# Kernel optimization log

Hardware: AMD Instinct MI355X
Metric: run time of the kernel (lower is better)

The kernel has to match this reference:

```python
import jax, jax.numpy as jnp
import numpy as np

D = 256      # d_model
H = 8        # n_heads
HD = D // H  # head_dim = 32
P = 16       # point dim per head


def setup_inputs() -> dict:
    key = jax.random.key(0)
    ks = jax.random.split(key, 12)
    B, S = 2, 2048
    w = lambda k, shape: jax.random.normal(k, shape, jnp.float32) * 0.02
    return {
        "seq_repr": jax.random.normal(ks[0], (B, S, D), jnp.float32),
        "coords": jax.random.normal(ks[1], (B, S, 3, 3), jnp.float32),
        "frames": jax.random.normal(ks[2], (B, S, 4), jnp.float32),
        "mask": jnp.ones((B, S), jnp.int32),
        "Wq": w(ks[3], (D, D)), "bq": jnp.zeros((D,), jnp.float32),
        "Wk": w(ks[4], (D, D)), "bk": jnp.zeros((D,), jnp.float32),
        "Wv": w(ks[5], (D, D)), "bv": jnp.zeros((D,), jnp.float32),
        "Wpq": w(ks[6], (3, H * P)), "bpq": jnp.zeros((H * P,), jnp.float32),
        "Wpk": w(ks[7], (3, H * P)), "bpk": jnp.zeros((H * P,), jnp.float32),
        "Wo": w(ks[8], (D, D)), "bo": jnp.zeros((D,), jnp.float32),
        "Wpo": w(ks[9], (H * P, 3)), "bpo": jnp.zeros((3,), jnp.float32),
        "attn_bias": jnp.zeros((H,), jnp.float32),
    }


def reference(seq_repr, coords, frames, mask, Wq, bq, Wk, bk, Wv, bv,
              Wpq, bpq, Wpk, bpk, Wo, bo, Wpo, bpo, attn_bias):
    B, S, _ = seq_repr.shape
    q = (seq_repr @ Wq + bq).reshape(B, S, H, HD)
    k = (seq_repr @ Wk + bk).reshape(B, S, H, HD)
    v = (seq_repr @ Wv + bv).reshape(B, S, H, HD)

    rep = coords[..., 1, :]                                  # [B,S,3] representative atom
    pq = (rep @ Wpq + bpq).reshape(B, S, H, P)
    pk = (rep @ Wpk + bpk).reshape(B, S, H, P)

    scale = 1.0 / np.sqrt(HD)
    scores = (jnp.einsum('bihd,bjhd->bhij', q, k) * scale
              + jnp.einsum('bihp,bjhp->bhij', pq, pk) * 0.25  # 1/sqrt(16)
              + attn_bias[None, :, None, None])

    mask2d = (mask[:, :, None] * mask[:, None, :])[:, None]  # [B,1,S,S]
    scores = jnp.where(mask2d == 0, jnp.float32(-1e9), scores)

    w = jax.nn.softmax(scores, axis=-1)                      # [B,H,S,S]

    seq_ctx = jnp.einsum('bhij,bjhd->bihd', w, v).reshape(B, S, D)
    pt_ctx = jnp.einsum('bhij,bjhp->bihp', w, pq).reshape(B, S, H * P)

    seq_out = seq_ctx @ Wo + bo                              # [B,S,D]
    point_out = pt_ctx @ Wpo + bpo                           # [B,S,3]
    return (seq_out, point_out)
```

## Files before the change

### kernel.cpp

```cpp
#include <hip/hip_runtime.h>
#include <hip/hip_bf16.h>

#define D_ 256
#define H_ 8
#define B_ 2
#define S_ 2048
#define MTOT 4096
#define AUGQ 64
#define NBH 16
#define KPAD 72
#define NJ 16

typedef __attribute__((ext_vector_type(8))) short short8;
typedef __attribute__((ext_vector_type(4))) short short4v;
typedef __attribute__((ext_vector_type(4))) float f32x4;

static __device__ __forceinline__ short bf16_of(float f) {
  union { __hip_bfloat16 h; short s; } u;
  u.h = __float2bfloat16(f);
  return u.s;
}
static __device__ __forceinline__ float f_of_bf16(short s) {
  union { float f; unsigned int u; } u;
  u.u = ((unsigned int)(unsigned short)s) << 16;
  return u.f;
}

static __device__ __forceinline__ f32x4 mfma16(short4v a, short4v b, f32x4 c) {
#if defined(__has_builtin) && __has_builtin(__builtin_amdgcn_mfma_f32_16x16x16bf16_1k)
  return __builtin_amdgcn_mfma_f32_16x16x16bf16_1k(a, b, c, 0, 0, 0);
#else
  asm("v_mfma_f32_16x16x16_bf16 %0, %1, %2, %0" : "+v"(c) : "v"(a), "v"(b));
  return c;
#endif
}


__global__ void prep_all(const float* __restrict__ Wq, const float* __restrict__ Wk,
                         const float* __restrict__ Wv, const float* __restrict__ Wo,
                         const float* __restrict__ coords, const int* __restrict__ mask,
                         const float* __restrict__ Wpq, const float* __restrict__ bpq,
                         const float* __restrict__ Wpk, const float* __restrict__ bpk,
                         short* __restrict__ Wqkv_t, short* __restrict__ Wo_t,
                         short* __restrict__ Qa, short* __restrict__ Ka,
                         short* __restrict__ VaT) {
  int gid = blockIdx.x * 256 + threadIdx.x;
  int NT = gridDim.x * 256;
  for (int idx = gid; idx < 768 * 256; idx += NT) {
    int n = idx >> 8, k = idx & 255;
    const float* W = (n < 256) ? Wq : (n < 512 ? Wk : Wv);
    Wqkv_t[idx] = bf16_of(W[k * 256 + (n & 255)]);
  }
  for (int idx = gid; idx < 256 * 256; idx += NT) {
    int n = idx >> 8, k = idx & 255;
    Wo_t[idx] = bf16_of(Wo[k * 256 + n]);
  }
  for (int idx = gid; idx < MTOT * 8; idx += NT) {
    int m = idx >> 3, h = idx & 7;
    int b = m >> 11, s = m & 2047;
    float r0 = coords[m * 9 + 3], r1 = coords[m * 9 + 4], r2 = coords[m * 9 + 5];
    size_t base = ((size_t)(b * 8 + h) * S_ + s) * AUGQ;
    short8 pqv[2], pkv[2];
#pragma unroll
    for (int c = 0; c < 2; c++)
#pragma unroll
      for (int i = 0; i < 8; i++) {
        int j = h * 16 + c * 8 + i;
        float pq = r0 * Wpq[j] + r1 * Wpq[128 + j] + r2 * Wpq[256 + j] + bpq[j];
        float pk = r0 * Wpk[j] + r1 * Wpk[128 + j] + r2 * Wpk[256 + j] + bpk[j];
        pqv[c][i] = bf16_of(pq);
        pkv[c][i] = bf16_of(pk * 0.25f);
      }
    short8 padq = {};
    padq[0] = 0x3F80;
    short8 padk = {};
    padk[0] = mask[m] ? (short)0 : bf16_of(-1e9f);
    short8 z = {};
    *reinterpret_cast<short8*>(&Qa[base + 32]) = pqv[0];
    *reinterpret_cast<short8*>(&Qa[base + 40]) = pqv[1];
    *reinterpret_cast<short8*>(&Qa[base + 48]) = padq;
    *reinterpret_cast<short8*>(&Qa[base + 56]) = z;
    *reinterpret_cast<short8*>(&Ka[base + 32]) = pkv[0];
    *reinterpret_cast<short8*>(&Ka[base + 40]) = pkv[1];
    *reinterpret_cast<short8*>(&Ka[base + 48]) = padk;
    *reinterpret_cast<short8*>(&Ka[base + 56]) = z;
  }
  for (int idx = gid; idx < NBH * 16 * (S_ / 8); idx += NT) {
    int s8 = idx & 255, p = (idx >> 8) & 15, bh = idx >> 12;
    int b = bh >> 3, h = bh & 7, j = h * 16 + p;
    float w0 = Wpq[j], w1 = Wpq[128 + j], w2 = Wpq[256 + j], bb = bpq[j];
    short8 o;
#pragma unroll
    for (int i = 0; i < 8; i++) {
      int m = b * 2048 + s8 * 8 + i;
      o[i] = bf16_of(coords[m * 9 + 3] * w0 + coords[m * 9 + 4] * w1 +
                     coords[m * 9 + 5] * w2 + bb);
    }
    *reinterpret_cast<short8*>(&VaT[((size_t)bh * 48 + 32 + p) * S_ + s8 * 8]) = o;
  }
}


__global__ __launch_bounds__(256) void qkv_gemm(
    const float* __restrict__ X, const short* __restrict__ Wt,
    const float* __restrict__ bq, const float* __restrict__ bk, const float* __restrict__ bv,
    short* __restrict__ Qa, short* __restrict__ Ka, short* __restrict__ VaT) {
  __shared__ __align__(16) short As[64 * 136];
  __shared__ __align__(16) short Bs[64 * 136];
  int m0 = blockIdx.x * 64, n0 = blockIdx.y * 64;
  int tid = threadIdx.x, lane = tid & 63, w = tid >> 6;
  int t = lane & 15, g = lane >> 4, kf = g * 8;
  int wr = (w >> 1) * 32, wc = (w & 1) * 32;
  f32x4 acc[2][2] = {};
  int srow = tid >> 2, skc = (tid & 3) * 32;
  for (int ph = 0; ph < 2; ph++) {
    int k0 = ph * 128;
    __syncthreads();
    {
      const float* xs = &X[(size_t)(m0 + srow) * 256 + k0 + skc];
      short4v av[8];
#pragma unroll
      for (int i = 0; i < 8; i++) {
        f32x4 xv = *reinterpret_cast<const f32x4*>(&xs[i * 4]);
        short4v o;
        o[0] = bf16_of(xv[0]); o[1] = bf16_of(xv[1]);
        o[2] = bf16_of(xv[2]); o[3] = bf16_of(xv[3]);
        av[i] = o;
      }
#pragma unroll
      for (int i = 0; i < 8; i++)
        *reinterpret_cast<short4v*>(&As[srow * 136 + skc + i * 4]) = av[i];
      const uint4* wsrc = reinterpret_cast<const uint4*>(&Wt[(size_t)(n0 + srow) * 256 + k0 + skc]);
#pragma unroll
      for (int i = 0; i < 4; i++)
        *reinterpret_cast<uint4*>(&Bs[srow * 136 + skc + i * 8]) = wsrc[i];
    }
    __syncthreads();
#pragma unroll
    for (int kk = 0; kk < 4; kk++) {
      short8 a[2], bb[2];
#pragma unroll
      for (int i = 0; i < 2; i++)
        a[i] = *reinterpret_cast<const short8*>(&As[(wr + i * 16 + t) * 136 + kk * 32 + kf]);
#pragma unroll
      for (int jj = 0; jj < 2; jj++)
        bb[jj] = *reinterpret_cast<const short8*>(&Bs[(wc + jj * 16 + t) * 136 + kk * 32 + kf]);
#pragma unroll
      for (int i = 0; i < 2; i++)
#pragma unroll
        for (int jj = 0; jj < 2; jj++)
          acc[i][jj] = __builtin_amdgcn_mfma_f32_16x16x32_bf16(a[i], bb[jj], acc[i][jj], 0, 0, 0);
    }
  }
  __syncthreads();
  short* Cs = As;
  const float scale = 0.17677669529663687f;
  int b = m0 >> 11, sbase = m0 & 2047;
#pragma unroll
  for (int i = 0; i < 2; i++)
#pragma unroll
    for (int jj = 0; jj < 2; jj++)
#pragma unroll
      for (int r = 0; r < 4; r++) {
        int rl = wr + i * 16 + g * 4 + r;
        int cl = wc + jj * 16 + t;
        int n = n0 + cl;
        float v = acc[i][jj][r];
        if (n < 256) v = (v + bq[n]) * scale;
        else if (n < 512) v = v + bk[n - 256];
        else v = v + bv[n - 512];
        Cs[rl * 72 + cl] = bf16_of(v);
      }
  __syncthreads();
  if (n0 < 512) {
#pragma unroll
    for (int i2 = 0; i2 < 2; i2++) {
      int task = tid + i2 * 256;
      int row = task >> 3, c = task & 7;
      int n = n0 + c * 8;
      short* dst = (n < 256) ? Qa : Ka;
      int nn = n & 255;
      int hh = nn >> 5, d = nn & 31;
      *reinterpret_cast<short8*>(&dst[((size_t)(b * 8 + hh) * S_ + sbase + row) * AUGQ + d]) =
          *reinterpret_cast<const short8*>(&Cs[row * 72 + c * 8]);
    }
  } else {
    int hv0 = (n0 - 512) >> 5;
#pragma unroll
    for (int i2 = 0; i2 < 2; i2++) {
      int task = tid + i2 * 256;
      int fl = task >> 3, s8 = task & 7;
      short8 o;
#pragma unroll
      for (int i = 0; i < 8; i++) o[i] = Cs[(s8 * 8 + i) * 72 + fl];
      int hh = hv0 + (fl >> 5), d = fl & 31;
      *reinterpret_cast<short8*>(&VaT[((size_t)(b * 8 + hh) * 48 + d) * S_ + sbase + s8 * 8]) = o;
    }
  }
}


__global__ __launch_bounds__(256, 4) void attn(
    const short* __restrict__ Qa, const short* __restrict__ Ka,
    const short* __restrict__ VaT,
    short* __restrict__ Ctx0, short* __restrict__ Ctx1,
    float* __restrict__ AccL) {
  __shared__ __align__(16) char smem[32256];

  int bid = blockIdx.x;
  int xcd = bid & 7, slot = bid >> 3;
  int gidx = xcd * 4 + (slot >> 5);
  int it = slot & 31;
  int split = gidx & 1;
  int bhv = gidx >> 1;

  int tid = threadIdx.x, lane = tid & 63, w = tid >> 6;
  int t = lane & 15, g = lane >> 4, kf = g * 8;
  int q0w = it * 64 + w * 16;
  size_t bh = (size_t)bhv * S_;

  short8 aq0 = *reinterpret_cast<const short8*>(&Qa[(bh + q0w + t) * AUGQ + kf]);
  short8 aq1 = *reinterpret_cast<const short8*>(&Qa[(bh + q0w + t) * AUGQ + 32 + kf]);

  f32x4 Oacc[3] = {};
  float lsum = 0.f;

  uint4 kreg0, kreg1, vreg0, vreg1;
  int srow = tid >> 3, sko = (tid & 7) * 8;
  const int jt0 = split * NJ;

  auto issue = [&](int jt) {
    const uint4* ks = reinterpret_cast<const uint4*>(&Ka[(bh + jt * 64) * AUGQ]);
    kreg0 = ks[tid];
    kreg1 = ks[tid + 256];
    size_t vb = (size_t)bhv * 48 * S_ + jt * 64;
    vreg0 = *reinterpret_cast<const uint4*>(&VaT[vb + (size_t)srow * S_ + sko]);
    if (tid < 128)
      vreg1 = *reinterpret_cast<const uint4*>(&VaT[vb + (size_t)(srow + 32) * S_ + sko]);
  };
  auto commit = [&](int buf) {
    short* Kd = (short*)(smem + buf * 9216);
    short* Vd = (short*)(smem + 18432 + buf * 6912);
    *reinterpret_cast<uint4*>(&Kd[srow * KPAD + sko]) = kreg0;
    *reinterpret_cast<uint4*>(&Kd[(srow + 32) * KPAD + sko]) = kreg1;
    *reinterpret_cast<uint4*>(&Vd[srow * KPAD + sko]) = vreg0;
    if (tid < 128)
      *reinterpret_cast<uint4*>(&Vd[(srow + 32) * KPAD + sko]) = vreg1;
  };

  issue(jt0);
  commit(0);
  __syncthreads();

  for (int j = 0; j < NJ; j++) {
    int cur = j & 1;
    if (j + 1 < NJ) issue(jt0 + j + 1);
    const short* Kc = (const short*)(smem + cur * 9216);
    const short* Vc = (const short*)(smem + 18432 + cur * 6912);
    short4v pb[4];
#pragma unroll
    for (int sub = 0; sub < 4; sub++) {
      short8 ka0 = *reinterpret_cast<const short8*>(&Kc[(sub * 16 + t) * KPAD + kf]);
      short8 ka1 = *reinterpret_cast<const short8*>(&Kc[(sub * 16 + t) * KPAD + 32 + kf]);
      f32x4 s0 = {};
      s0 = __builtin_amdgcn_mfma_f32_16x16x32_bf16(ka0, aq0, s0, 0, 0, 0);
      s0 = __builtin_amdgcn_mfma_f32_16x16x32_bf16(ka1, aq1, s0, 0, 0, 0);
      float p0 = __expf(s0[0]);
      float p1 = __expf(s0[1]);
      float p2 = __expf(s0[2]);
      float p3 = __expf(s0[3]);
      lsum += (p0 + p1) + (p2 + p3);
      short4v pk4;
      pk4[0] = bf16_of(p0); pk4[1] = bf16_of(p1);
      pk4[2] = bf16_of(p2); pk4[3] = bf16_of(p3);
      pb[sub] = pk4;
    }
#pragma unroll
    for (int tt = 0; tt < 3; tt++) {
#pragma unroll
      for (int sub = 0; sub < 4; sub++) {
        short4v va = *reinterpret_cast<const short4v*>(&Vc[(tt * 16 + t) * KPAD + sub * 16 + g * 4]);
        Oacc[tt] = mfma16(va, pb[sub], Oacc[tt]);
      }
    }
    if (j + 1 < NJ) commit(cur ^ 1);
    __syncthreads();
  }

  lsum += __shfl_xor(lsum, 16);
  lsum += __shfl_xor(lsum, 32);

  float* Of = (float*)smem;
#pragma unroll
  for (int tt = 0; tt < 3; tt++)
#pragma unroll
    for (int r = 0; r < 4; r++)
      Of[(w * 16 + t) * 52 + tt * 16 + g * 4 + r] = Oacc[tt][r];
  if (lane < 16) AccL[(size_t)(split * NBH + bhv) * S_ + q0w + lane] = lsum;
  __syncthreads();
  short* CtxP = split ? Ctx1 : Ctx0;
  size_t obase = bh + it * 64;
  for (int task = tid; task < 384; task += 256) {
    int row = task / 6, c8 = task % 6;
    const float* src = &Of[row * 52 + c8 * 8];
    short8 o;
#pragma unroll
    for (int i = 0; i < 8; i++) o[i] = bf16_of(src[i]);
    *reinterpret_cast<short8*>(&CtxP[(obase + row) * 48 + c8 * 8]) = o;
  }
}


__global__ __launch_bounds__(512) void out_gemm(
    const short* __restrict__ Ctx0, const short* __restrict__ Ctx1,
    const float* __restrict__ AccL,
    const short* __restrict__ Wot, const float* __restrict__ bo,
    float* __restrict__ Out) {
  __shared__ __align__(16) short As[64 * 136];
  __shared__ __align__(16) short Bs[64 * 136];
  int m0 = blockIdx.x * 64, n0 = blockIdx.y * 64;
  int tid = threadIdx.x, lane = tid & 63, w = tid >> 6;
  int t = lane & 15, g = lane >> 4, kf = g * 8;
  int wm = w & 3, wn = w >> 2;
  int b = m0 >> 11, sbase = m0 & 2047;
  f32x4 acc[2] = {};
  int srow = tid >> 3, skc = (tid & 7) * 16;
  for (int ph = 0; ph < 2; ph++) {
    int k0 = ph * 128;
    __syncthreads();
    {
      int kg = k0 + skc;
      int hh = kg >> 5, d0 = kg & 31;
      size_t rowO = (size_t)(b * 8 + hh) * S_ + sbase + srow;
      float inv = 1.0f / (AccL[rowO] + AccL[rowO + (size_t)NBH * S_]);
      const short8* c0 = reinterpret_cast<const short8*>(&Ctx0[rowO * 48 + d0]);
      const short8* c1 = reinterpret_cast<const short8*>(&Ctx1[rowO * 48 + d0]);
#pragma unroll
      for (int half = 0; half < 2; half++) {
        short8 a0 = c0[half], a1 = c1[half];
        short8 o;
#pragma unroll
        for (int c = 0; c < 8; c++)
          o[c] = bf16_of((f_of_bf16(a0[c]) + f_of_bf16(a1[c])) * inv);
        *reinterpret_cast<short8*>(&As[srow * 136 + skc + half * 8]) = o;
      }
      *reinterpret_cast<uint4*>(&Bs[srow * 136 + skc]) =
          *reinterpret_cast<const uint4*>(&Wot[(size_t)(n0 + srow) * 256 + kg]);
      *reinterpret_cast<uint4*>(&Bs[srow * 136 + skc + 8]) =
          *reinterpret_cast<const uint4*>(&Wot[(size_t)(n0 + srow) * 256 + kg + 8]);
    }
    __syncthreads();
#pragma unroll
    for (int kk = 0; kk < 4; kk++) {
      short8 a = *reinterpret_cast<const short8*>(&As[(wm * 16 + t) * 136 + kk * 32 + kf]);
#pragma unroll
      for (int jj = 0; jj < 2; jj++) {
        short8 bb = *reinterpret_cast<const short8*>(&Bs[(wn * 32 + jj * 16 + t) * 136 + kk * 32 + kf]);
        acc[jj] = __builtin_amdgcn_mfma_f32_16x16x32_bf16(a, bb, acc[jj], 0, 0, 0);
      }
    }
  }
#pragma unroll
  for (int jj = 0; jj < 2; jj++)
#pragma unroll
    for (int r = 0; r < 4; r++) {
      int mrow = m0 + wm * 16 + g * 4 + r;
      int n = n0 + wn * 32 + jj * 16 + t;
      Out[(size_t)mrow * 256 + n] = acc[jj][r] + bo[n];
    }
}


__global__ void point_proj(const short* __restrict__ Ctx0, const short* __restrict__ Ctx1,
                           const float* __restrict__ AccL,
                           const float* __restrict__ Wpo, const float* __restrict__ bpo,
                           float* __restrict__ out) {
  int gid = blockIdx.x * 256 + threadIdx.x;
  int m = gid >> 2, qr = gid & 3;
  int b = m >> 11, s = m & 2047;
  float a0 = 0.f, a1 = 0.f, a2 = 0.f;
#pragma unroll
  for (int h2 = 0; h2 < 2; h2++) {
    int hh = qr * 2 + h2;
    size_t rowO = (size_t)(b * 8 + hh) * S_ + s;
    float inv = 1.0f / (AccL[rowO] + AccL[rowO + (size_t)NBH * S_]);
    const short8* c0 = reinterpret_cast<const short8*>(&Ctx0[rowO * 48 + 32]);
    const short8* c1 = reinterpret_cast<const short8*>(&Ctx1[rowO * 48 + 32]);
#pragma unroll
    for (int half = 0; half < 2; half++) {
      short8 v0 = c0[half], v1 = c1[half];
#pragma unroll
      for (int c = 0; c < 8; c++) {
        float val = (f_of_bf16(v0[c]) + f_of_bf16(v1[c])) * inv;
        int j = hh * 16 + half * 8 + c;
        a0 += val * Wpo[j * 3 + 0];
        a1 += val * Wpo[j * 3 + 1];
        a2 += val * Wpo[j * 3 + 2];
      }
    }
  }
  a0 += __shfl_xor(a0, 1); a0 += __shfl_xor(a0, 2);
  a1 += __shfl_xor(a1, 1); a1 += __shfl_xor(a1, 2);
  a2 += __shfl_xor(a2, 1); a2 += __shfl_xor(a2, 2);
  if (qr == 0) {
    out[(size_t)m * 3 + 0] = a0 + bpo[0];
    out[(size_t)m * 3 + 1] = a1 + bpo[1];
    out[(size_t)m * 3 + 2] = a2 + bpo[2];
  }
}


extern "C" void kernel_launch(void* const* d_in, const int* in_sizes, int n_in,
                              void* d_out, int out_size, void* d_ws, size_t ws_size,
                              hipStream_t stream) {
  const float* seq    = (const float*)d_in[0];
  const float* coords = (const float*)d_in[1];
  const int*   mask   = (const int*)d_in[3];
  const float* Wq  = (const float*)d_in[4];
  const float* bq  = (const float*)d_in[5];
  const float* Wk  = (const float*)d_in[6];
  const float* bk  = (const float*)d_in[7];
  const float* Wv  = (const float*)d_in[8];
  const float* bv  = (const float*)d_in[9];
  const float* Wpq = (const float*)d_in[10];
  const float* bpq = (const float*)d_in[11];
  const float* Wpk = (const float*)d_in[12];
  const float* bpk = (const float*)d_in[13];
  const float* Wo  = (const float*)d_in[14];
  const float* bo  = (const float*)d_in[15];
  const float* Wpo = (const float*)d_in[16];
  const float* bpo = (const float*)d_in[17];
  float* out = (float*)d_out;

  char* ws = (char*)d_ws;
  short* Wqkv_t = (short*)ws; ws += 768 * 256 * 2;
  short* Wo_t   = (short*)ws; ws += 256 * 256 * 2;
  short* Qa     = (short*)ws; ws += (size_t)NBH * S_ * AUGQ * 2;
  short* Ka     = (short*)ws; ws += (size_t)NBH * S_ * AUGQ * 2;
  short* VaT    = (short*)ws; ws += (size_t)NBH * 48 * S_ * 2;
  short* Ctx0   = (short*)ws; ws += (size_t)NBH * S_ * 48 * 2;
  short* Ctx1   = (short*)ws; ws += (size_t)NBH * S_ * 48 * 2;
  float* AccL   = (float*)ws; ws += (size_t)2 * NBH * S_ * 4;

  prep_all<<<1024, 256, 0, stream>>>(Wq, Wk, Wv, Wo, coords, mask, Wpq, bpq, Wpk, bpk,
                                     Wqkv_t, Wo_t, Qa, Ka, VaT);
  qkv_gemm<<<dim3(64, 12), 256, 0, stream>>>(seq, Wqkv_t, bq, bk, bv, Qa, Ka, VaT);
  attn<<<1024, 256, 0, stream>>>(Qa, Ka, VaT, Ctx0, Ctx1, AccL);
  out_gemm<<<dim3(64, 4), 512, 0, stream>>>(Ctx0, Ctx1, AccL, Wo_t, bo, out);
  point_proj<<<64, 256, 0, stream>>>(Ctx0, Ctx1, AccL, Wpo, bpo, out + (size_t)MTOT * 256);
}
```

Baseline: 69.38 us.

## Split attention keys four ways, single-buffer LDS, and use exp2 with log2e folding

Raises the key-dimension split of the attention kernel from two to four, doubling the grid to 2048 blocks with half the key tiles each. LDS double buffering becomes a single buffer with an extra barrier, halving shared memory so occupancy can rise to eight blocks per CU. Log2(e) is folded into the Q scale, the point-query projection and the bias column so the kernel can call exp2f instead of __expf, and s_setprio is raised around the PV MFMAs. The out_gemm and point_proj kernels now reduce four partial contexts and sums, which adds epilogue memory traffic and removes the overlap of global loads with compute.

```diff
diff --git a/kernel.cpp b/kernel.cpp
--- a/kernel.cpp
+++ b/kernel.cpp
@@ -9,7 +9,9 @@
 #define AUGQ 64
 #define NBH 16
 #define KPAD 72
-#define NJ 16
+#define NSPLIT 4
+#define NJ 8
+#define LOG2E 1.4426950408889634f
 
 typedef __attribute__((ext_vector_type(8))) short short8;
 typedef __attribute__((ext_vector_type(4))) short short4v;
@@ -68,11 +70,11 @@
         int j = h * 16 + c * 8 + i;
         float pq = r0 * Wpq[j] + r1 * Wpq[128 + j] + r2 * Wpq[256 + j] + bpq[j];
         float pk = r0 * Wpk[j] + r1 * Wpk[128 + j] + r2 * Wpk[256 + j] + bpk[j];
-        pqv[c][i] = bf16_of(pq);
+        pqv[c][i] = bf16_of(pq * LOG2E);
         pkv[c][i] = bf16_of(pk * 0.25f);
       }
     short8 padq = {};
-    padq[0] = 0x3F80;
+    padq[0] = bf16_of(LOG2E);
     short8 padk = {};
     padk[0] = mask[m] ? (short)0 : bf16_of(-1e9f);
     short8 z = {};
@@ -154,7 +156,7 @@
   }
   __syncthreads();
   short* Cs = As;
-  const float scale = 0.17677669529663687f;
+  const float scale = 0.17677669529663687f * LOG2E;
   int b = m0 >> 11, sbase = m0 & 2047;
 #pragma unroll
   for (int i = 0; i < 2; i++)
@@ -200,19 +202,18 @@
 }
 
 
-__global__ __launch_bounds__(256, 4) void attn(
+__global__ __launch_bounds__(256, 8) void attn(
     const short* __restrict__ Qa, const short* __restrict__ Ka,
     const short* __restrict__ VaT,
-    short* __restrict__ Ctx0, short* __restrict__ Ctx1,
-    float* __restrict__ AccL) {
-  __shared__ __align__(16) char smem[32256];
+    short* __restrict__ Ctx, float* __restrict__ AccL) {
+  __shared__ __align__(16) char smem[16128];
 
   int bid = blockIdx.x;
   int xcd = bid & 7, slot = bid >> 3;
-  int gidx = xcd * 4 + (slot >> 5);
+  int gidx = xcd * 8 + (slot >> 5);
   int it = slot & 31;
-  int split = gidx & 1;
-  int bhv = gidx >> 1;
+  int split = gidx & 3;
+  int bhv = gidx >> 2;
 
   int tid = threadIdx.x, lane = tid & 63, w = tid >> 6;
   int t = lane & 15, g = lane >> 4, kf = g * 8;
@@ -238,9 +239,9 @@
     if (tid < 128)
       vreg1 = *reinterpret_cast<const uint4*>(&VaT[vb + (size_t)(srow + 32) * S_ + sko]);
   };
-  auto commit = [&](int buf) {
-    short* Kd = (short*)(smem + buf * 9216);
-    short* Vd = (short*)(smem + 18432 + buf * 6912);
+  auto commit = [&]() {
+    short* Kd = (short*)smem;
+    short* Vd = (short*)(smem + 9216);
     *reinterpret_cast<uint4*>(&Kd[srow * KPAD + sko]) = kreg0;
     *reinterpret_cast<uint4*>(&Kd[(srow + 32) * KPAD + sko]) = kreg1;
     *reinterpret_cast<uint4*>(&Vd[srow * KPAD + sko]) = vreg0;
@@ -249,14 +250,13 @@
   };
 
   issue(jt0);
-  commit(0);
+  commit();
   __syncthreads();
 
+  const short* Kc = (const short*)smem;
+  const short* Vc = (const short*)(smem + 9216);
   for (int j = 0; j < NJ; j++) {
-    int cur = j & 1;
     if (j + 1 < NJ) issue(jt0 + j + 1);
-    const short* Kc = (const short*)(smem + cur * 9216);
-    const short* Vc = (const short*)(smem + 18432 + cur * 6912);
     short4v pb[4];
 #pragma unroll
     for (int sub = 0; sub < 4; sub++) {
@@ -265,16 +265,17 @@
       f32x4 s0 = {};
       s0 = __builtin_amdgcn_mfma_f32_16x16x32_bf16(ka0, aq0, s0, 0, 0, 0);
       s0 = __builtin_amdgcn_mfma_f32_16x16x32_bf16(ka1, aq1, s0, 0, 0, 0);
-      float p0 = __expf(s0[0]);
-      float p1 = __expf(s0[1]);
-      float p2 = __expf(s0[2]);
-      float p3 = __expf(s0[3]);
+      float p0 = exp2f(s0[0]);
+      float p1 = exp2f(s0[1]);
+      float p2 = exp2f(s0[2]);
+      float p3 = exp2f(s0[3]);
       lsum += (p0 + p1) + (p2 + p3);
       short4v pk4;
       pk4[0] = bf16_of(p0); pk4[1] = bf16_of(p1);
       pk4[2] = bf16_of(p2); pk4[3] = bf16_of(p3);
       pb[sub] = pk4;
     }
+    __builtin_amdgcn_s_setprio(1);
 #pragma unroll
     for (int tt = 0; tt < 3; tt++) {
 #pragma unroll
@@ -283,8 +284,12 @@
         Oacc[tt] = mfma16(va, pb[sub], Oacc[tt]);
       }
     }
-    if (j + 1 < NJ) commit(cur ^ 1);
+    __builtin_amdgcn_s_setprio(0);
     __syncthreads();
+    if (j + 1 < NJ) {
+      commit();
+      __syncthreads();
+    }
   }
 
   lsum += __shfl_xor(lsum, 16);
@@ -298,7 +303,7 @@
       Of[(w * 16 + t) * 52 + tt * 16 + g * 4 + r] = Oacc[tt][r];
   if (lane < 16) AccL[(size_t)(split * NBH + bhv) * S_ + q0w + lane] = lsum;
   __syncthreads();
-  short* CtxP = split ? Ctx1 : Ctx0;
+  short* CtxP = Ctx + (size_t)split * NBH * S_ * 48;
   size_t obase = bh + it * 64;
   for (int task = tid; task < 384; task += 256) {
     int row = task / 6, c8 = task % 6;
@@ -312,12 +317,12 @@
 
 
 __global__ __launch_bounds__(512) void out_gemm(
-    const short* __restrict__ Ctx0, const short* __restrict__ Ctx1,
-    const float* __restrict__ AccL,
+    const short* __restrict__ Ctx, const float* __restrict__ AccL,
     const short* __restrict__ Wot, const float* __restrict__ bo,
     float* __restrict__ Out) {
   __shared__ __align__(16) short As[64 * 136];
   __shared__ __align__(16) short Bs[64 * 136];
+  const size_t CTXSZ = (size_t)NBH * S_ * 48;
   int m0 = blockIdx.x * 64, n0 = blockIdx.y * 64;
   int tid = threadIdx.x, lane = tid & 63, w = tid >> 6;
   int t = lane & 15, g = lane >> 4, kf = g * 8;
@@ -332,16 +337,22 @@
       int kg = k0 + skc;
       int hh = kg >> 5, d0 = kg & 31;
       size_t rowO = (size_t)(b * 8 + hh) * S_ + sbase + srow;
-      float inv = 1.0f / (AccL[rowO] + AccL[rowO + (size_t)NBH * S_]);
-      const short8* c0 = reinterpret_cast<const short8*>(&Ctx0[rowO * 48 + d0]);
-      const short8* c1 = reinterpret_cast<const short8*>(&Ctx1[rowO * 48 + d0]);
+      float l = 0.f;
+#pragma unroll
+      for (int sp = 0; sp < NSPLIT; sp++) l += AccL[(size_t)sp * NBH * S_ + rowO];
+      float inv = 1.0f / l;
 #pragma unroll
       for (int half = 0; half < 2; half++) {
-        short8 a0 = c0[half], a1 = c1[half];
+        float sum[8] = {};
+#pragma unroll
+        for (int sp = 0; sp < NSPLIT; sp++) {
+          short8 a = *reinterpret_cast<const short8*>(&Ctx[sp * CTXSZ + rowO * 48 + d0 + half * 8]);
+#pragma unroll
+          for (int c = 0; c < 8; c++) sum[c] += f_of_bf16(a[c]);
+        }
         short8 o;
 #pragma unroll
-        for (int c = 0; c < 8; c++)
-          o[c] = bf16_of((f_of_bf16(a0[c]) + f_of_bf16(a1[c])) * inv);
+        for (int c = 0; c < 8; c++) o[c] = bf16_of(sum[c] * inv);
         *reinterpret_cast<short8*>(&As[srow * 136 + skc + half * 8]) = o;
       }
       *reinterpret_cast<uint4*>(&Bs[srow * 136 + skc]) =
@@ -371,10 +382,10 @@
 }
 
 
-__global__ void point_proj(const short* __restrict__ Ctx0, const short* __restrict__ Ctx1,
-                           const float* __restrict__ AccL,
+__global__ void point_proj(const short* __restrict__ Ctx, const float* __restrict__ AccL,
                            const float* __restrict__ Wpo, const float* __restrict__ bpo,
                            float* __restrict__ out) {
+  const size_t CTXSZ = (size_t)NBH * S_ * 48;
   int gid = blockIdx.x * 256 + threadIdx.x;
   int m = gid >> 2, qr = gid & 3;
   int b = m >> 11, s = m & 2047;
@@ -383,15 +394,22 @@
   for (int h2 = 0; h2 < 2; h2++) {
     int hh = qr * 2 + h2;
     size_t rowO = (size_t)(b * 8 + hh) * S_ + s;
-    float inv = 1.0f / (AccL[rowO] + AccL[rowO + (size_t)NBH * S_]);
-    const short8* c0 = reinterpret_cast<const short8*>(&Ctx0[rowO * 48 + 32]);
-    const short8* c1 = reinterpret_cast<const short8*>(&Ctx1[rowO * 48 + 32]);
+    float l = 0.f;
+#pragma unroll
+    for (int sp = 0; sp < NSPLIT; sp++) l += AccL[(size_t)sp * NBH * S_ + rowO];
+    float inv = 1.0f / l;
 #pragma unroll
     for (int half = 0; half < 2; half++) {
-      short8 v0 = c0[half], v1 = c1[half];
+      float sum[8] = {};
+#pragma unroll
+      for (int sp = 0; sp < NSPLIT; sp++) {
+        short8 v = *reinterpret_cast<const short8*>(&Ctx[sp * CTXSZ + rowO * 48 + 32 + half * 8]);
+#pragma unroll
+        for (int c = 0; c < 8; c++) sum[c] += f_of_bf16(v[c]);
+      }
 #pragma unroll
       for (int c = 0; c < 8; c++) {
-        float val = (f_of_bf16(v0[c]) + f_of_bf16(v1[c])) * inv;
+        float val = sum[c] * inv;
         int j = hh * 16 + half * 8 + c;
         a0 += val * Wpo[j * 3 + 0];
         a1 += val * Wpo[j * 3 + 1];
@@ -438,14 +456,13 @@
   short* Qa     = (short*)ws; ws += (size_t)NBH * S_ * AUGQ * 2;
   short* Ka     = (short*)ws; ws += (size_t)NBH * S_ * AUGQ * 2;
   short* VaT    = (short*)ws; ws += (size_t)NBH * 48 * S_ * 2;
-  short* Ctx0   = (short*)ws; ws += (size_t)NBH * S_ * 48 * 2;
-  short* Ctx1   = (short*)ws; ws += (size_t)NBH * S_ * 48 * 2;
-  float* AccL   = (float*)ws; ws += (size_t)2 * NBH * S_ * 4;
+  short* Ctx    = (short*)ws; ws += (size_t)NSPLIT * NBH * S_ * 48 * 2;
+  float* AccL   = (float*)ws; ws += (size_t)NSPLIT * NBH * S_ * 4;
 
   prep_all<<<1024, 256, 0, stream>>>(Wq, Wk, Wv, Wo, coords, mask, Wpq, bpq, Wpk, bpk,
                                      Wqkv_t, Wo_t, Qa, Ka, VaT);
   qkv_gemm<<<dim3(64, 12), 256, 0, stream>>>(seq, Wqkv_t, bq, bk, bv, Qa, Ka, VaT);
-  attn<<<1024, 256, 0, stream>>>(Qa, Ka, VaT, Ctx0, Ctx1, AccL);
-  out_gemm<<<dim3(64, 4), 512, 0, stream>>>(Ctx0, Ctx1, AccL, Wo_t, bo, out);
-  point_proj<<<64, 256, 0, stream>>>(Ctx0, Ctx1, AccL, Wpo, bpo, out + (size_t)MTOT * 256);
-}
+  attn<<<2048, 256, 0, stream>>>(Qa, Ka, VaT, Ctx, AccL);
+  out_gemm<<<dim3(64, 4), 512, 0, stream>>>(Ctx, AccL, Wo_t, bo, out);
+  point_proj<<<64, 256, 0, stream>>>(Ctx, AccL, Wpo, bpo, out + (size_t)MTOT * 256);
+}
```

Measured after the change: 116.1 us. 67.4% more time.

## Double queries per attention wave, fold log2e into Q, merge point projection

Applied to the files above, without the earlier changes.

Each attention wave now handles 32 query rows instead of 16, so every K/V tile in shared memory is reused across two query groups and the grid halves to 512 blocks with launch bounds relaxed to two blocks per CU. log2(e) is folded into the Q scale and the point/bias columns so exp2f can replace __expf. MFMA priority is raised during the PV phase. The separate point_proj kernel is merged into out_gemm as an extra grid column to save a launch. The cost is higher register pressure and fewer resident blocks, which may hurt latency hiding.

```diff
diff --git a/kernel.cpp b/kernel.cpp
--- a/kernel.cpp
+++ b/kernel.cpp
@@ -9,7 +9,9 @@
 #define AUGQ 64
 #define NBH 16
 #define KPAD 72
+#define NSPLIT 2
 #define NJ 16
+#define LOG2E 1.4426950408889634f
 
 typedef __attribute__((ext_vector_type(8))) short short8;
 typedef __attribute__((ext_vector_type(4))) short short4v;
@@ -68,11 +70,11 @@
         int j = h * 16 + c * 8 + i;
         float pq = r0 * Wpq[j] + r1 * Wpq[128 + j] + r2 * Wpq[256 + j] + bpq[j];
         float pk = r0 * Wpk[j] + r1 * Wpk[128 + j] + r2 * Wpk[256 + j] + bpk[j];
-        pqv[c][i] = bf16_of(pq);
+        pqv[c][i] = bf16_of(pq * LOG2E);
         pkv[c][i] = bf16_of(pk * 0.25f);
       }
     short8 padq = {};
-    padq[0] = 0x3F80;
+    padq[0] = bf16_of(LOG2E);
     short8 padk = {};
     padk[0] = mask[m] ? (short)0 : bf16_of(-1e9f);
     short8 z = {};
@@ -154,7 +156,7 @@
   }
   __syncthreads();
   short* Cs = As;
-  const float scale = 0.17677669529663687f;
+  const float scale = 0.17677669529663687f * LOG2E;
   int b = m0 >> 11, sbase = m0 & 2047;
 #pragma unroll
   for (int i = 0; i < 2; i++)
@@ -200,30 +202,34 @@
 }
 
 
-__global__ __launch_bounds__(256, 4) void attn(
+__global__ __launch_bounds__(256, 2) void attn(
     const short* __restrict__ Qa, const short* __restrict__ Ka,
     const short* __restrict__ VaT,
-    short* __restrict__ Ctx0, short* __restrict__ Ctx1,
-    float* __restrict__ AccL) {
+    short* __restrict__ Ctx, float* __restrict__ AccL) {
   __shared__ __align__(16) char smem[32256];
 
   int bid = blockIdx.x;
   int xcd = bid & 7, slot = bid >> 3;
-  int gidx = xcd * 4 + (slot >> 5);
-  int it = slot & 31;
+  int gidx = xcd * 4 + (slot >> 4);
+  int it = slot & 15;
   int split = gidx & 1;
   int bhv = gidx >> 1;
 
   int tid = threadIdx.x, lane = tid & 63, w = tid >> 6;
   int t = lane & 15, g = lane >> 4, kf = g * 8;
-  int q0w = it * 64 + w * 16;
+  int q0w = it * 128 + w * 32;
   size_t bh = (size_t)bhv * S_;
 
-  short8 aq0 = *reinterpret_cast<const short8*>(&Qa[(bh + q0w + t) * AUGQ + kf]);
-  short8 aq1 = *reinterpret_cast<const short8*>(&Qa[(bh + q0w + t) * AUGQ + 32 + kf]);
-
-  f32x4 Oacc[3] = {};
-  float lsum = 0.f;
+  short8 aq[2][2];
+#pragma unroll
+  for (int g2 = 0; g2 < 2; g2++)
+#pragma unroll
+    for (int c = 0; c < 2; c++)
+      aq[g2][c] = *reinterpret_cast<const short8*>(
+          &Qa[(bh + q0w + g2 * 16 + t) * AUGQ + c * 32 + kf]);
+
+  f32x4 OaccA[3] = {}, OaccB[3] = {};
+  float lsum0 = 0.f, lsum1 = 0.f;
 
   uint4 kreg0, kreg1, vreg0, vreg1;
   int srow = tid >> 3, sko = (tid & 7) * 8;
@@ -257,50 +263,60 @@
     if (j + 1 < NJ) issue(jt0 + j + 1);
     const short* Kc = (const short*)(smem + cur * 9216);
     const short* Vc = (const short*)(smem + 18432 + cur * 6912);
-    short4v pb[4];
+    short4v pbA[4], pbB[4];
 #pragma unroll
     for (int sub = 0; sub < 4; sub++) {
       short8 ka0 = *reinterpret_cast<const short8*>(&Kc[(sub * 16 + t) * KPAD + kf]);
       short8 ka1 = *reinterpret_cast<const short8*>(&Kc[(sub * 16 + t) * KPAD + 32 + kf]);
-      f32x4 s0 = {};
-      s0 = __builtin_amdgcn_mfma_f32_16x16x32_bf16(ka0, aq0, s0, 0, 0, 0);
-      s0 = __builtin_amdgcn_mfma_f32_16x16x32_bf16(ka1, aq1, s0, 0, 0, 0);
-      float p0 = __expf(s0[0]);
-      float p1 = __expf(s0[1]);
-      float p2 = __expf(s0[2]);
-      float p3 = __expf(s0[3]);
-      lsum += (p0 + p1) + (p2 + p3);
-      short4v pk4;
-      pk4[0] = bf16_of(p0); pk4[1] = bf16_of(p1);
-      pk4[2] = bf16_of(p2); pk4[3] = bf16_of(p3);
-      pb[sub] = pk4;
-    }
+      f32x4 sA = {}, sB = {};
+      sA = __builtin_amdgcn_mfma_f32_16x16x32_bf16(ka0, aq[0][0], sA, 0, 0, 0);
+      sA = __builtin_amdgcn_mfma_f32_16x16x32_bf16(ka1, aq[0][1], sA, 0, 0, 0);
+      sB = __builtin_amdgcn_mfma_f32_16x16x32_bf16(ka0, aq[1][0], sB, 0, 0, 0);
+      sB = __builtin_amdgcn_mfma_f32_16x16x32_bf16(ka1, aq[1][1], sB, 0, 0, 0);
+      float a0 = exp2f(sA[0]), a1 = exp2f(sA[1]), a2 = exp2f(sA[2]), a3 = exp2f(sA[3]);
+      float b0 = exp2f(sB[0]), b1 = exp2f(sB[1]), b2 = exp2f(sB[2]), b3 = exp2f(sB[3]);
+      lsum0 += (a0 + a1) + (a2 + a3);
+      lsum1 += (b0 + b1) + (b2 + b3);
+      short4v pa, pb;
+      pa[0] = bf16_of(a0); pa[1] = bf16_of(a1); pa[2] = bf16_of(a2); pa[3] = bf16_of(a3);
+      pb[0] = bf16_of(b0); pb[1] = bf16_of(b1); pb[2] = bf16_of(b2); pb[3] = bf16_of(b3);
+      pbA[sub] = pa; pbB[sub] = pb;
+    }
+    __builtin_amdgcn_s_setprio(1);
 #pragma unroll
     for (int tt = 0; tt < 3; tt++) {
 #pragma unroll
       for (int sub = 0; sub < 4; sub++) {
         short4v va = *reinterpret_cast<const short4v*>(&Vc[(tt * 16 + t) * KPAD + sub * 16 + g * 4]);
-        Oacc[tt] = mfma16(va, pb[sub], Oacc[tt]);
-      }
-    }
+        OaccA[tt] = mfma16(va, pbA[sub], OaccA[tt]);
+        OaccB[tt] = mfma16(va, pbB[sub], OaccB[tt]);
+      }
+    }
+    __builtin_amdgcn_s_setprio(0);
     if (j + 1 < NJ) commit(cur ^ 1);
     __syncthreads();
   }
 
-  lsum += __shfl_xor(lsum, 16);
-  lsum += __shfl_xor(lsum, 32);
+  lsum0 += __shfl_xor(lsum0, 16); lsum0 += __shfl_xor(lsum0, 32);
+  lsum1 += __shfl_xor(lsum1, 16); lsum1 += __shfl_xor(lsum1, 32);
 
   float* Of = (float*)smem;
 #pragma unroll
   for (int tt = 0; tt < 3; tt++)
 #pragma unroll
-    for (int r = 0; r < 4; r++)
-      Of[(w * 16 + t) * 52 + tt * 16 + g * 4 + r] = Oacc[tt][r];
-  if (lane < 16) AccL[(size_t)(split * NBH + bhv) * S_ + q0w + lane] = lsum;
+    for (int r = 0; r < 4; r++) {
+      Of[(w * 32 + t) * 52 + tt * 16 + g * 4 + r] = OaccA[tt][r];
+      Of[(w * 32 + 16 + t) * 52 + tt * 16 + g * 4 + r] = OaccB[tt][r];
+    }
+  if (lane < 16) {
+    size_t lb = (size_t)(split * NBH + bhv) * S_ + q0w + lane;
+    AccL[lb] = lsum0;
+    AccL[lb + 16] = lsum1;
+  }
   __syncthreads();
-  short* CtxP = split ? Ctx1 : Ctx0;
-  size_t obase = bh + it * 64;
-  for (int task = tid; task < 384; task += 256) {
+  short* CtxP = Ctx + (size_t)split * NBH * S_ * 48;
+  size_t obase = bh + it * 128;
+  for (int task = tid; task < 768; task += 256) {
     int row = task / 6, c8 = task % 6;
     const float* src = &Of[row * 52 + c8 * 8];
     short8 o;
@@ -312,17 +328,52 @@
 
 
 __global__ __launch_bounds__(512) void out_gemm(
-    const short* __restrict__ Ctx0, const short* __restrict__ Ctx1,
-    const float* __restrict__ AccL,
+    const short* __restrict__ Ctx, const float* __restrict__ AccL,
     const short* __restrict__ Wot, const float* __restrict__ bo,
+    const float* __restrict__ Wpo, const float* __restrict__ bpo,
     float* __restrict__ Out) {
+  const size_t CTXSZ = (size_t)NBH * S_ * 48;
+  int m0 = blockIdx.x * 64;
+  int tid = threadIdx.x;
+  int b = m0 >> 11, sbase = m0 & 2047;
+
+  if (blockIdx.y == 4) {
+    int row = tid >> 3, hh = tid & 7;
+    int m = m0 + row, s = sbase + row;
+    size_t rowO = (size_t)(b * 8 + hh) * S_ + s;
+    float inv = 1.0f / (AccL[rowO] + AccL[(size_t)NBH * S_ + rowO]);
+    float a0 = 0.f, a1 = 0.f, a2 = 0.f;
+#pragma unroll
+    for (int half = 0; half < 2; half++) {
+      short8 v0 = *reinterpret_cast<const short8*>(&Ctx[rowO * 48 + 32 + half * 8]);
+      short8 v1 = *reinterpret_cast<const short8*>(&Ctx[CTXSZ + rowO * 48 + 32 + half * 8]);
+#pragma unroll
+      for (int c = 0; c < 8; c++) {
+        float val = (f_of_bf16(v0[c]) + f_of_bf16(v1[c])) * inv;
+        int j = hh * 16 + half * 8 + c;
+        a0 += val * Wpo[j * 3 + 0];
+        a1 += val * Wpo[j * 3 + 1];
+        a2 += val * Wpo[j * 3 + 2];
+      }
+    }
+    a0 += __shfl_xor(a0, 1); a0 += __shfl_xor(a0, 2); a0 += __shfl_xor(a0, 4);
+    a1 += __shfl_xor(a1, 1); a1 += __shfl_xor(a1, 2); a1 += __shfl_xor(a1, 4);
+    a2 += __shfl_xor(a2, 1); a2 += __shfl_xor(a2, 2); a2 += __shfl_xor(a2, 4);
+    if (hh == 0) {
+      float* po = Out + (size_t)MTOT * 256;
+      po[(size_t)m * 3 + 0] = a0 + bpo[0];
+      po[(size_t)m * 3 + 1] = a1 + bpo[1];
+      po[(size_t)m * 3 + 2] = a2 + bpo[2];
+    }
+    return;
+  }
+
   __shared__ __align__(16) short As[64 * 136];
   __shared__ __align__(16) short Bs[64 * 136];
-  int m0 = blockIdx.x * 64, n0 = blockIdx.y * 64;
-  int tid = threadIdx.x, lane = tid & 63, w = tid >> 6;
+  int n0 = blockIdx.y * 64;
+  int lane = tid & 63, w = tid >> 6;
   int t = lane & 15, g = lane >> 4, kf = g * 8;
   int wm = w & 3, wn = w >> 2;
-  int b = m0 >> 11, sbase = m0 & 2047;
   f32x4 acc[2] = {};
   int srow = tid >> 3, skc = (tid & 7) * 16;
   for (int ph = 0; ph < 2; ph++) {
@@ -332,12 +383,11 @@
       int kg = k0 + skc;
       int hh = kg >> 5, d0 = kg & 31;
       size_t rowO = (size_t)(b * 8 + hh) * S_ + sbase + srow;
-      float inv = 1.0f / (AccL[rowO] + AccL[rowO + (size_t)NBH * S_]);
-      const short8* c0 = reinterpret_cast<const short8*>(&Ctx0[rowO * 48 + d0]);
-      const short8* c1 = reinterpret_cast<const short8*>(&Ctx1[rowO * 48 + d0]);
+      float inv = 1.0f / (AccL[rowO] + AccL[(size_t)NBH * S_ + rowO]);
 #pragma unroll
       for (int half = 0; half < 2; half++) {
-        short8 a0 = c0[half], a1 = c1[half];
+        short8 a0 = *reinterpret_cast<const short8*>(&Ctx[rowO * 48 + d0 + half * 8]);
+        short8 a1 = *reinterpret_cast<const short8*>(&Ctx[CTXSZ + rowO * 48 + d0 + half * 8]);
         short8 o;
 #pragma unroll
         for (int c = 0; c < 8; c++)
@@ -368,45 +418,6 @@
       int n = n0 + wn * 32 + jj * 16 + t;
       Out[(size_t)mrow * 256 + n] = acc[jj][r] + bo[n];
     }
-}
-
-
-__global__ void point_proj(const short* __restrict__ Ctx0, const short* __restrict__ Ctx1,
-                           const float* __restrict__ AccL,
-                           const float* __restrict__ Wpo, const float* __restrict__ bpo,
-                           float* __restrict__ out) {
-  int gid = blockIdx.x * 256 + threadIdx.x;
-  int m = gid >> 2, qr = gid & 3;
-  int b = m >> 11, s = m & 2047;
-  float a0 = 0.f, a1 = 0.f, a2 = 0.f;
-#pragma unroll
-  for (int h2 = 0; h2 < 2; h2++) {
-    int hh = qr * 2 + h2;
-    size_t rowO = (size_t)(b * 8 + hh) * S_ + s;
-    float inv = 1.0f / (AccL[rowO] + AccL[rowO + (size_t)NBH * S_]);
-    const short8* c0 = reinterpret_cast<const short8*>(&Ctx0[rowO * 48 + 32]);
-    const short8* c1 = reinterpret_cast<const short8*>(&Ctx1[rowO * 48 + 32]);
-#pragma unroll
-    for (int half = 0; half < 2; half++) {
-      short8 v0 = c0[half], v1 = c1[half];
-#pragma unroll
-      for (int c = 0; c < 8; c++) {
-        float val = (f_of_bf16(v0[c]) + f_of_bf16(v1[c])) * inv;
-        int j = hh * 16 + half * 8 + c;
-        a0 += val * Wpo[j * 3 + 0];
-        a1 += val * Wpo[j * 3 + 1];
-        a2 += val * Wpo[j * 3 + 2];
-      }
-    }
-  }
-  a0 += __shfl_xor(a0, 1); a0 += __shfl_xor(a0, 2);
-  a1 += __shfl_xor(a1, 1); a1 += __shfl_xor(a1, 2);
-  a2 += __shfl_xor(a2, 1); a2 += __shfl_xor(a2, 2);
-  if (qr == 0) {
-    out[(size_t)m * 3 + 0] = a0 + bpo[0];
-    out[(size_t)m * 3 + 1] = a1 + bpo[1];
-    out[(size_t)m * 3 + 2] = a2 + bpo[2];
-  }
 }
 
 
@@ -438,14 +449,12 @@
   short* Qa     = (short*)ws; ws += (size_t)NBH * S_ * AUGQ * 2;
   short* Ka     = (short*)ws; ws += (size_t)NBH * S_ * AUGQ * 2;
   short* VaT    = (short*)ws; ws += (size_t)NBH * 48 * S_ * 2;
-  short* Ctx0   = (short*)ws; ws += (size_t)NBH * S_ * 48 * 2;
-  short* Ctx1   = (short*)ws; ws += (size_t)NBH * S_ * 48 * 2;
-  float* AccL   = (float*)ws; ws += (size_t)2 * NBH * S_ * 4;
+  short* Ctx    = (short*)ws; ws += (size_t)NSPLIT * NBH * S_ * 48 * 2;
+  float* AccL   = (float*)ws; ws += (size_t)NSPLIT * NBH * S_ * 4;
 
   prep_all<<<1024, 256, 0, stream>>>(Wq, Wk, Wv, Wo, coords, mask, Wpq, bpq, Wpk, bpk,
                                      Wqkv_t, Wo_t, Qa, Ka, VaT);
   qkv_gemm<<<dim3(64, 12), 256, 0, stream>>>(seq, Wqkv_t, bq, bk, bv, Qa, Ka, VaT);
-  attn<<<1024, 256, 0, stream>>>(Qa, Ka, VaT, Ctx0, Ctx1, AccL);
-  out_gemm<<<dim3(64, 4), 512, 0, stream>>>(Ctx0, Ctx1, AccL, Wo_t, bo, out);
-  point_proj<<<64, 256, 0, stream>>>(Ctx0, Ctx1, AccL, Wpo, bpo, out + (size_t)MTOT * 256);
-}
+  attn<<<512, 256, 0, stream>>>(Qa, Ka, VaT, Ctx, AccL);
+  out_gemm<<<dim3(64, 5), 512, 0, stream>>>(Ctx, AccL, Wo_t, bo, Wpo, bpo, out);
+}
```

New measurement: 69.52 us. About the same (+0.2%).
